# Performance work log

Measured on AMD Instinct MI355X. Metric: run time of the kernel, lower is better.

## Reference

```python
import jax, jax.numpy as jnp
import numpy as np

FEAT_STRIDE = 16
ANCHOR_SCALES = (8.0, 16.0, 32.0)
ANCHOR_RATIOS = (0.5, 1.0, 2.0)
NUM_ANCHORS = 9
PRE_NMS_TOP_N = 12000
POST_NMS_TOP_N = 300
NMS_THRESH = 0.7
POOLING_SIZE = 7
RPN_NEG_OVERLAP = 0.3
RPN_POS_OVERLAP = 0.7


def _generate_base_anchors(base_size=16):
    ratios = np.array(ANCHOR_RATIOS)
    scales = np.array(ANCHOR_SCALES)
    ctr = (base_size - 1) / 2.0
    size = float(base_size * base_size)
    ws = np.round(np.sqrt(size / ratios))
    hs = np.round(ws * ratios)
    ws = (ws[:, None] * scales[None, :]).ravel()  # order (ratio, scale)
    hs = (hs[:, None] * scales[None, :]).ravel()
    return np.stack([ctr - 0.5 * (ws - 1), ctr - 0.5 * (hs - 1),
                     ctr + 0.5 * (ws - 1), ctr + 0.5 * (hs - 1)], axis=1)


def _all_anchors(H, W):
    base = _generate_base_anchors()  # (A,4)
    sx = np.arange(W) * FEAT_STRIDE
    sy = np.arange(H) * FEAT_STRIDE
    sx, sy = np.meshgrid(sx, sy)  # (H,W)
    shifts = np.stack([sx.ravel(), sy.ravel(), sx.ravel(), sy.ravel()], axis=1)  # (H*W,4)
    anchors = (shifts[:, None, :] + base[None, :, :]).reshape(-1, 4)  # order (h,w,a)
    return jnp.asarray(anchors, dtype=jnp.float32)


def _conv(x, w, b):
    y = jax.lax.conv_general_dilated(x, w, (1, 1), 'SAME',
                                     dimension_numbers=('NCHW', 'OIHW', 'NCHW'))
    return y + b[None, :, None, None]


def _decode(anchors, deltas):
    w = anchors[:, 2] - anchors[:, 0] + 1.0
    h = anchors[:, 3] - anchors[:, 1] + 1.0
    cx = anchors[:, 0] + 0.5 * w
    cy = anchors[:, 1] + 0.5 * h
    pcx = deltas[:, 0] * w + cx
    pcy = deltas[:, 1] * h + cy
    pw = jnp.exp(deltas[:, 2]) * w
    ph = jnp.exp(deltas[:, 3]) * h
    return jnp.stack([pcx - 0.5 * pw, pcy - 0.5 * ph, pcx + 0.5 * pw, pcy + 0.5 * ph], axis=1)


def _encode(ex, gt):
    ew = ex[:, 2] - ex[:, 0] + 1.0
    eh = ex[:, 3] - ex[:, 1] + 1.0
    ecx = ex[:, 0] + 0.5 * ew
    ecy = ex[:, 1] + 0.5 * eh
    gw = gt[:, 2] - gt[:, 0] + 1.0
    gh = gt[:, 3] - gt[:, 1] + 1.0
    gcx = gt[:, 0] + 0.5 * gw
    gcy = gt[:, 1] + 0.5 * gh
    return jnp.stack([(gcx - ecx) / ew, (gcy - ecy) / eh,
                      jnp.log(gw / ew), jnp.log(gh / eh)], axis=1)


def _clip_boxes(b, im_h, im_w):
    return jnp.stack([jnp.clip(b[:, 0], 0.0, im_w - 1.0),
                      jnp.clip(b[:, 1], 0.0, im_h - 1.0),
                      jnp.clip(b[:, 2], 0.0, im_w - 1.0),
                      jnp.clip(b[:, 3], 0.0, im_h - 1.0)], axis=1)


def _iou_matrix(a, b):
    aa = (a[:, 2] - a[:, 0] + 1.0) * (a[:, 3] - a[:, 1] + 1.0)
    ba = (b[:, 2] - b[:, 0] + 1.0) * (b[:, 3] - b[:, 1] + 1.0)
    x1 = jnp.maximum(a[:, None, 0], b[None, :, 0])
    y1 = jnp.maximum(a[:, None, 1], b[None, :, 1])
    x2 = jnp.minimum(a[:, None, 2], b[None, :, 2])
    y2 = jnp.minimum(a[:, None, 3], b[None, :, 3])
    inter = jnp.maximum(x2 - x1 + 1.0, 0.0) * jnp.maximum(y2 - y1 + 1.0, 0.0)
    return inter / (aa[:, None] + ba[None, :] - inter)


def _nms(boxes, thresh, max_out):
    # boxes (N,4) already sorted by score descending; greedy NMS, fixed output size
    areas = (boxes[:, 2] - boxes[:, 0] + 1.0) * (boxes[:, 3] - boxes[:, 1] + 1.0)
    N = boxes.shape[0]

    def body(i, state):
        valid, keep = state
        idx = jnp.argmax(valid)  # first still-valid (highest score)
        has = valid[idx]
        b = boxes[idx]
        xx1 = jnp.maximum(b[0], boxes[:, 0])
        yy1 = jnp.maximum(b[1], boxes[:, 1])
        xx2 = jnp.minimum(b[2], boxes[:, 2])
        yy2 = jnp.minimum(b[3], boxes[:, 3])
        inter = jnp.maximum(xx2 - xx1 + 1.0, 0.0) * jnp.maximum(yy2 - yy1 + 1.0, 0.0)
        iou = inter / (areas[idx] + areas - inter)
        valid = jnp.where(has, valid & (iou <= thresh), valid)
        keep = keep.at[i].set(jnp.where(has, idx, 0).astype(jnp.int32))
        return valid, keep

    valid0 = jnp.ones((N,), dtype=bool)
    keep0 = jnp.zeros((max_out,), dtype=jnp.int32)
    _, keep = jax.lax.fori_loop(0, max_out, body, (valid0, keep0))
    return keep


def _roi_crop(feat, rois, P):
    # affine_grid + grid_sample (align_corners=True, zero padding), matching STRPN.pooling
    C, H, W = feat.shape[1], feat.shape[2], feat.shape[3]
    f = feat[0].reshape(C, H * W)
    R = rois.shape[0]
    x1 = rois[:, 1] / 16.0
    y1 = rois[:, 2] / 16.0
    x2 = rois[:, 3] / 16.0
    y2 = rois[:, 4] / 16.0
    t00 = (x2 - x1) / (W - 1)
    t02 = (x1 + x2 - W + 1) / (W - 1)
    t11 = (y2 - y1) / (H - 1)
    t12 = (y1 + y2 - H + 1) / (H - 1)
    lin = jnp.linspace(-1.0, 1.0, P)
    gx = jnp.broadcast_to(t00[:, None, None] * lin[None, None, :] + t02[:, None, None], (R, P, P))
    gy = jnp.broadcast_to(t11[:, None, None] * lin[None, :, None] + t12[:, None, None], (R, P, P))
    ix = (gx + 1.0) * 0.5 * (W - 1)
    iy = (gy + 1.0) * 0.5 * (H - 1)
    ix0 = jnp.floor(ix)
    iy0 = jnp.floor(iy)
    wx = ix - ix0
    wy = iy - iy0

    def gather(yi, xi, wgt):
        valid = (yi >= 0) & (yi < H) & (xi >= 0) & (xi < W)
        yc = jnp.clip(yi, 0, H - 1).astype(jnp.int32)
        xc = jnp.clip(xi, 0, W - 1).astype(jnp.int32)
        v = f[:, yc * W + xc]  # (C,R,P,P)
        return v * (wgt * valid)[None]

    out = (gather(iy0, ix0, (1 - wy) * (1 - wx)) + gather(iy0, ix0 + 1, (1 - wy) * wx)
           + gather(iy0 + 1, ix0, wy * (1 - wx)) + gather(iy0 + 1, ix0 + 1, wy * wx))
    return jnp.transpose(out, (1, 0, 2, 3))  # (R,C,P,P)


def _anchor_targets(anchors, gt_boxes, im_h, im_w):
    inside = ((anchors[:, 0] >= 0) & (anchors[:, 1] >= 0)
              & (anchors[:, 2] < im_w) & (anchors[:, 3] < im_h))
    ov = _iou_matrix(anchors, gt_boxes[:, :4])
    ov = jnp.where(inside[:, None], ov, -1.0)
    max_ov = ov.max(axis=1)
    argmax = ov.argmax(axis=1)
    gt_max = ov.max(axis=0)  # (G,)
    is_best = (ov == gt_max[None, :]).any(axis=1)
    labels = jnp.full(anchors.shape[:1], -1.0, dtype=jnp.float32)
    labels = jnp.where(inside & (max_ov < RPN_NEG_OVERLAP), 0.0, labels)
    labels = jnp.where(inside & is_best, 1.0, labels)
    labels = jnp.where(inside & (max_ov >= RPN_POS_OVERLAP), 1.0, labels)
    targets = _encode(anchors, gt_boxes[argmax, :4])
    pos = (labels == 1.0)
    ex = (labels >= 0.0)
    n_ex = jnp.maximum(ex.sum(), 1).astype(jnp.float32)
    in_w = pos[:, None].astype(jnp.float32)
    out_w = ex[:, None].astype(jnp.float32) / n_ex
    return labels, targets, in_w, out_w


def _forward(head_features, gt_boxes, im_info, rpn_w, rpn_b, cls_w, cls_b, bbox_w, bbox_b):
    A = NUM_ANCHORS
    H, W = head_features.shape[2], head_features.shape[3]
    anchors = _all_anchors(H, W)  # order (h,w,a)
    rpn = jax.nn.relu(_conv(head_features, rpn_w, rpn_b))
    cls_score = _conv(rpn, cls_w, cls_b)[0]   # (2A,H,W); channel layout cls*A + a
    bbox_pred = _conv(rpn, bbox_w, bbox_b)[0]  # (4A,H,W); channel layout a*4 + coord
    cls2 = cls_score.reshape(2, A, H, W)
    fg = jax.nn.softmax(cls2, axis=0)[1]  # (A,H,W)
    scores = jnp.transpose(fg, (1, 2, 0)).reshape(-1)  # (h,w,a)
    deltas = jnp.transpose(bbox_pred.reshape(A, 4, H, W), (2, 3, 0, 1)).reshape(-1, 4)
    im_h, im_w = im_info[0], im_info[1]
    proposals = _clip_boxes(_decode(anchors, deltas), im_h, im_w)
    _, order = jax.lax.top_k(scores, PRE_NMS_TOP_N)
    props = proposals[order]
    keep = _nms(props, NMS_THRESH, POST_NMS_TOP_N)
    sel = props[keep]
    rois = jnp.concatenate([jnp.zeros((POST_NMS_TOP_N, 1), sel.dtype), sel], axis=1)
    # RPN losses (anchor targets are numpy/constants in the original => stop_gradient)
    labels, tgt, iw, ow = jax.tree_util.tree_map(
        jax.lax.stop_gradient, _anchor_targets(anchors, gt_boxes, im_h, im_w))
    logits = jnp.transpose(cls2, (2, 3, 1, 0)).reshape(-1, 2)  # (h,w,a,2)
    logp = jax.nn.log_softmax(logits, axis=-1)
    mask = (labels >= 0).astype(logp.dtype)
    lbl = jnp.clip(labels, 0.0, 1.0).astype(jnp.int32)
    ce = -jnp.take_along_axis(logp, lbl[:, None], axis=1)[:, 0]
    cls_loss = jnp.sum(ce * mask) / jnp.maximum(mask.sum(), 1.0)
    sigma2 = 9.0  # sigma=3
    diff = iw * (deltas - tgt)
    ad = jnp.abs(diff)
    flag = (ad < 1.0 / sigma2).astype(diff.dtype)
    sl1 = flag * 0.5 * sigma2 * diff * diff + (1.0 - flag) * (ad - 0.5 / sigma2)
    box_loss = jnp.sum(ow * sl1)  # batch=1: sum over dims == mean over batch of per-image sums
    pooled = _roi_crop(head_features, jax.lax.stop_gradient(rois), POOLING_SIZE)
    return pooled, cls_loss, box_loss


def setup_inputs() -> dict:
    key = jax.random.key(0)
    ks = jax.random.split(key, 10)
    head_features = jax.random.normal(ks[0], (1, 1024, 96, 96), jnp.float32)
    G = 8
    x1 = jax.random.uniform(ks[1], (G,), minval=0.0, maxval=1100.0)
    y1 = jax.random.uniform(ks[2], (G,), minval=0.0, maxval=1000.0)
    bw = jax.random.uniform(ks[3], (G,), minval=50.0, maxval=300.0)
    bh = jax.random.uniform(ks[4], (G,), minval=100.0, maxval=450.0)
    gt_boxes = jnp.stack([x1, y1, jnp.minimum(x1 + bw, 1535.0),
                          jnp.minimum(y1 + bh, 1535.0), jnp.ones((G,))], axis=1).astype(jnp.float32)
    im_info = jnp.array([1536.0, 1536.0, 1.0], jnp.float32)
    rpn_w = jax.random.normal(ks[5], (512, 1024, 3, 3), jnp.float32) * 0.01
    rpn_b = jnp.zeros((512,), jnp.float32)
    cls_w = jax.random.normal(ks[6], (18, 512, 1, 1), jnp.float32) * 0.01
    cls_b = jnp.zeros((18,), jnp.float32)
    bbox_w = jax.random.normal(ks[7], (36, 512, 1, 1), jnp.float32) * 0.01
    bbox_b = jnp.zeros((36,), jnp.float32)
    return {"head_features": head_features, "gt_boxes": gt_boxes, "im_info": im_info,
            "rpn_w": rpn_w, "rpn_b": rpn_b, "cls_w": cls_w, "cls_b": cls_b,
            "bbox_w": bbox_w, "bbox_b": bbox_b}


def reference(head_features, gt_boxes, im_info, rpn_w, rpn_b, cls_w, cls_b, bbox_w, bbox_b):
    return _forward(head_features, gt_boxes, im_info, rpn_w, rpn_b, cls_w, cls_b, bbox_w, bbox_b)
```

## Files before the change

### kernel.cpp

```cpp
#include <hip/hip_runtime.h>
#include <stdint.h>

typedef unsigned int u32;
typedef unsigned long long u64;
typedef _Float16 f16x8 __attribute__((ext_vector_type(8)));
typedef float f32x4 __attribute__((ext_vector_type(4)));

#define HF 96
#define HW 9216
#define CIN 1024
#define CMID 512
#define NA 82944
#define PRE 12000
#define POST 300
#define NW 188
#define NBLK 324
#define OUT_POOL (POST*CIN*49)

__device__ __constant__ float BA[9][4] = {
  {-84.f,-40.f,99.f,55.f}, {-176.f,-88.f,191.f,103.f}, {-360.f,-184.f,375.f,199.f},
  {-56.f,-56.f,71.f,71.f}, {-120.f,-120.f,135.f,135.f}, {-248.f,-248.f,263.f,263.f},
  {-36.f,-80.f,51.f,95.f}, {-80.f,-168.f,95.f,183.f},  {-168.f,-344.f,183.f,359.f}
};

__device__ __forceinline__ u32 fkey(float f) {
  u32 u = __float_as_uint(f);
  return (u & 0x80000000u) ? ~u : (u | 0x80000000u);
}

__device__ __forceinline__ void gl_lds16(const void* g, void* l) {
  __builtin_amdgcn_global_load_lds((const __attribute__((address_space(1))) void*)g,
                                   (__attribute__((address_space(3))) void*)l, 16, 0, 0);
}

__global__ void prep_img(const float* __restrict__ feat, f16x8* __restrict__ img)
{
  __shared__ float ls[32][100];
  const int yy = blockIdx.x;
  const int kt = blockIdx.y;
  const int tid = threadIdx.x;
  const int y = yy - 1;
  const bool yok = (unsigned)y < 96u;
  if (yok) {
    for (int e = tid; e < 3072; e += 256) {
      const int ci = e / 96;
      const int x = e - ci * 96;
      ls[ci][x] = feat[(size_t)(kt*32 + ci)*HW + y*96 + x];
    }
  }
  __syncthreads();
  for (int idx = tid; idx < 784; idx += 256) {
    const int col = idx >> 3;
    const int q = idx & 7;
    const int x = col - 1;
    f16x8 val;
#pragma unroll
    for (int i=0;i<8;i++) val[i] = (_Float16)0.f;
    if (yok && (unsigned)x < 96u) {
#pragma unroll
      for (int i=0;i<8;i++) {
        const float v = ls[(q&3)*8 + i][x];
        if (q < 4) val[i] = (_Float16)v;
        else { const _Float16 hi = (_Float16)v; val[i] = (_Float16)((v - (float)hi)*1024.f); }
      }
    }
    const int sw = (col + 2*y) & 7;
    img[(size_t)((kt*98 + yy)*98 + col)*8 + (q ^ sw)] = val;
  }
}

__global__ void prep_w(const float* __restrict__ w, f16x8* __restrict__ wbuf)
{
  const int t = blockIdx.x*256 + threadIdx.x;
  const int co = t & 511;
  const int cic = t >> 9;
  const int kt = cic >> 2;
  const int kg = cic & 3;
  const float* wp = w + (size_t)co*9216 + cic*72;
#pragma unroll
  for (int tap=0; tap<9; ++tap) {
    f16x8 hv, lv;
#pragma unroll
    for (int i=0;i<8;i++) {
      const float v = wp[i*9 + tap] * 64.f;
      const _Float16 hi = (_Float16)v;
      hv[i] = hi;
      lv[i] = (_Float16)((v - (float)hi)*1024.f);
    }
    wbuf[(size_t)(((kt*9 + tap)*2 + 0)*4 + kg)*512 + co] = hv;
    wbuf[(size_t)(((kt*9 + tap)*2 + 1)*4 + kg)*512 + co] = lv;
  }
}

__global__ __launch_bounds__(128, 2) void rpn_conv_mfma(
    const f16x8* __restrict__ img, const f16x8* __restrict__ wbuf,
    const float* __restrict__ bias, float* __restrict__ out)
{
  __shared__ f16x8 in_s[2560];
  const int tid = threadIdx.x;
  const int lane = tid & 63;
  const int wv = tid >> 6;
  const int kgrp = lane >> 4;
  const int ln15 = lane & 15;
  const int x0 = blockIdx.x * 48;
  const int y  = blockIdx.y;
  const int co0 = blockIdx.z * 128 + wv * 64;

  int goff[10];
#pragma unroll
  for (int j=0;j<10;j++) {
    int s = j*128 + tid; if (s > 1199) s = 1199;
    const int row = s / 400;
    const int rem = s - row*400;
    goff[j] = ((y + row)*98 + x0 + (rem>>3))*8 + (rem & 7);
  }
  const int ldst0 = wv*64;

  int keyb[3];
#pragma unroll
  for (int pt=0; pt<3; ++pt) keyb[pt] = x0 + pt*16 + ln15 + 1 + 2*y;

  f32x4 acc1[4][3], acc2[4][3];
#pragma unroll
  for (int c=0;c<4;c++)
#pragma unroll
    for (int pt=0;pt<3;pt++) {
      acc1[c][pt] = (f32x4){0.f,0.f,0.f,0.f};
      acc2[c][pt] = (f32x4){0.f,0.f,0.f,0.f};
    }

  const int wlane = kgrp*512 + co0 + ln15;

#pragma unroll
  for (int j=0;j<10;j++) gl_lds16(img + goff[j], in_s + j*128 + ldst0);
  asm volatile("s_waitcnt vmcnt(0)" ::: "memory");
  __syncthreads();

  for (int kt = 0; kt < 32; ++kt) {
    const int cur = (kt & 1) * 1280;
    if (kt < 31) {
      const f16x8* kb = img + (size_t)(kt+1)*76832;
#pragma unroll
      for (int j=0;j<10;j++) gl_lds16(kb + goff[j], in_s + (1280 - cur) + j*128 + ldst0);
    }
    const f16x8* bs = in_s + cur;
#pragma unroll
    for (int t=0; t<9; ++t) {
      const int dy = t/3 - 1, dx = t%3 - 1;
      f16x8 af[4][2];
#pragma unroll
      for (int h=0;h<2;h++) {
        const size_t wb = (size_t)(((kt*9 + t)*2 + h)*2048) + wlane;
#pragma unroll
        for (int c=0;c<4;c++) af[c][h] = wbuf[wb + c*16];
      }
      f16x8 bf[3][2];
#pragma unroll
      for (int pt=0;pt<3;pt++) {
        const int key = (keyb[pt] + dx + 2*dy) & 7;
        const int base = ((dy+1)*50 + pt*16 + ln15 + dx + 1)*8;
#pragma unroll
        for (int h=0;h<2;h++)
          bf[pt][h] = bs[base + ((h*4 + kgrp) ^ key)];
      }
#pragma unroll
      for (int c=0;c<4;c++)
#pragma unroll
        for (int pt=0;pt<3;pt++) {
          acc1[c][pt] = __builtin_amdgcn_mfma_f32_16x16x32_f16(af[c][0], bf[pt][0], acc1[c][pt], 0,0,0);
          acc2[c][pt] = __builtin_amdgcn_mfma_f32_16x16x32_f16(af[c][0], bf[pt][1], acc2[c][pt], 0,0,0);
          acc2[c][pt] = __builtin_amdgcn_mfma_f32_16x16x32_f16(af[c][1], bf[pt][0], acc2[c][pt], 0,0,0);
        }
    }
    asm volatile("s_waitcnt vmcnt(0)" ::: "memory");
    __syncthreads();
  }

  const int pixb = y*96 + x0;
#pragma unroll
  for (int c=0;c<4;c++) {
#pragma unroll
    for (int i=0;i<4;i++) {
      const int co = co0 + c*16 + kgrp*4 + i;
      const float bb = bias[co];
#pragma unroll
      for (int pt=0;pt<3;pt++) {
        const float v = (acc1[c][pt][i] + acc2[c][pt][i]*(1.f/1024.f))*(1.f/64.f) + bb;
        out[(size_t)co*HW + pixb + pt*16 + ln15] = v > 0.f ? v : 0.f;
      }
    }
  }
}

__global__ void conv1x1p(const float* __restrict__ rpn,
    const float* __restrict__ cw, const float* __restrict__ bw,
    float* __restrict__ partial)
{
  const int hw = blockIdx.x * 256 + threadIdx.x;
  const int cg = blockIdx.y;
  const int ci0 = cg * 64;
  float accA[18], accB[36];
#pragma unroll
  for (int c=0;c<18;c++) accA[c]=0.f;
#pragma unroll
  for (int c=0;c<36;c++) accB[c]=0.f;
  for (int ci=ci0; ci<ci0+64; ++ci) {
    const float v = rpn[(size_t)ci*HW + hw];
#pragma unroll
    for (int c=0;c<18;c++) accA[c] = fmaf(v, cw[c*CMID+ci], accA[c]);
#pragma unroll
    for (int c=0;c<36;c++) accB[c] = fmaf(v, bw[c*CMID+ci], accB[c]);
  }
  float* p = partial + (size_t)cg*54*HW;
#pragma unroll
  for (int c=0;c<18;c++) p[(size_t)c*HW + hw] = accA[c];
#pragma unroll
  for (int c=0;c<36;c++) p[(size_t)(18+c)*HW + hw] = accB[c];
}

__global__ void conv1x1r(const float* __restrict__ partial,
    const float* __restrict__ cb, const float* __restrict__ bb,
    float* __restrict__ cls_out, float* __restrict__ bbox_out)
{
  const int o = blockIdx.x*256 + threadIdx.x;
  const int c = o / HW;
  const int hw = o - c*HW;
  float v = partial[o];
#pragma unroll
  for (int g=1; g<8; ++g) v += partial[(size_t)g*54*HW + o];
  if (c < 18) cls_out[(size_t)c*HW + hw] = v + cb[c];
  else        bbox_out[(size_t)(c-18)*HW + hw] = v + bb[c-18];
}

__global__ void score_decode_ov(const float* __restrict__ cls_out,
    const float* __restrict__ bbox_out, const float* __restrict__ im_info,
    const float* __restrict__ gt,
    u64* __restrict__ keys, float4* __restrict__ props, u32* __restrict__ hist10,
    float* __restrict__ ov, u32* __restrict__ gtmax)
{
#pragma clang fp contract(off)
  __shared__ u32 h[1024];
  __shared__ u32 lmax[8];
  const int tid = threadIdx.x;
  for (int i=tid;i<1024;i+=256) h[i]=0;
  if (tid < 8) lmax[tid] = 0u;
  __syncthreads();
  const int n = blockIdx.x*256 + tid;
  const int hw = n / 9;
  const int a  = n - hw*9;
  const int x = hw % HF, y = hw / HF;
  const float l0 = cls_out[a*HW + hw];
  const float l1 = cls_out[(9+a)*HW + hw];
  const float m = fmaxf(l0, l1);
  const float e0 = expf(l0 - m), e1 = expf(l1 - m);
  const float s = e1 / (e0 + e1);
  const u32 sb = __float_as_uint(s);
  keys[n] = ((u64)(~sb) << 32) | (u32)n;
  atomicAdd(&h[sb >> 22], 1u);

  const float ax1 = BA[a][0] + 16.f*(float)x;
  const float ay1 = BA[a][1] + 16.f*(float)y;
  const float ax2 = BA[a][2] + 16.f*(float)x;
  const float ay2 = BA[a][3] + 16.f*(float)y;
  const float aw = ax2 - ax1 + 1.f, ah = ay2 - ay1 + 1.f;
  const float cx = ax1 + 0.5f*aw,  cy = ay1 + 0.5f*ah;
  const float d0 = bbox_out[(a*4+0)*HW + hw];
  const float d1 = bbox_out[(a*4+1)*HW + hw];
  const float d2 = bbox_out[(a*4+2)*HW + hw];
  const float d3 = bbox_out[(a*4+3)*HW + hw];
  const float pcx = d0*aw + cx, pcy = d1*ah + cy;
  const float pw = expf(d2)*aw, ph = expf(d3)*ah;
  const float imh = im_info[0], imw = im_info[1];
  float bx1 = fminf(fmaxf(pcx - 0.5f*pw, 0.f), imw - 1.f);
  float by1 = fminf(fmaxf(pcy - 0.5f*ph, 0.f), imh - 1.f);
  float bx2 = fminf(fmaxf(pcx + 0.5f*pw, 0.f), imw - 1.f);
  float by2 = fminf(fmaxf(pcy + 0.5f*ph, 0.f), imh - 1.f);
  props[n] = make_float4(bx1, by1, bx2, by2);

  const bool inside = (ax1 >= 0.f) && (ay1 >= 0.f) && (ax2 < imw) && (ay2 < imh);
  const float aa = aw * ah;
#pragma unroll
  for (int j=0;j<8;j++) {
    const float g0=gt[j*5+0], g1=gt[j*5+1], g2=gt[j*5+2], g3=gt[j*5+3];
    const float ga = (g2-g0+1.f)*(g3-g1+1.f);
    const float xx1 = fmaxf(ax1,g0), yy1 = fmaxf(ay1,g1);
    const float xx2 = fminf(ax2,g2), yy2 = fminf(ay2,g3);
    const float inter = fmaxf(xx2-xx1+1.f,0.f)*fmaxf(yy2-yy1+1.f,0.f);
    const float iou = inter/(aa+ga-inter);
    const float o = inside ? iou : -1.f;
    ov[(size_t)n*8+j] = o;
    atomicMax(&lmax[j], fkey(o));
  }
  __syncthreads();
  for (int i=tid;i<1024;i+=256) if (h[i]) atomicAdd(&hist10[i], h[i]);
  if (tid < 8) atomicMax(&gtmax[tid], lmax[tid]);
}

__global__ void hist_scan1(const u32* __restrict__ hist10, u32* __restrict__ meta)
{
  __shared__ u32 c[1024];
  const int t = threadIdx.x;
  c[t] = hist10[t];
  __syncthreads();
  if (t == 0) {
    u32 cum = 0;
    int b = 1023;
    for (; b > 0; --b) {
      if (cum + c[b] >= PRE) break;
      cum += c[b];
    }
    meta[0] = (u32)b;
    meta[1] = cum;
  }
}

__global__ void refine_label(const u64* __restrict__ keys, const u32* __restrict__ meta,
                             u32* __restrict__ h64,
                             const float* __restrict__ ov, const u32* __restrict__ gtmax,
                             signed char* __restrict__ labels, signed char* __restrict__ amax,
                             int* __restrict__ exP)
{
  __shared__ u32 h[64];
  __shared__ int se[256];
  const int tid = threadIdx.x;
  if (tid < 64) h[tid] = 0;
  __syncthreads();
  const int n = blockIdx.x*256 + tid;
  const u32 sb = ~(u32)(keys[n] >> 32);
  if ((sb >> 22) == meta[0]) atomicAdd(&h[(sb >> 16) & 63], 1u);

  float best = -3.402823466e38f;
  int arg = 0;
  bool isbest = false;
#pragma unroll
  for (int j=0;j<8;j++) {
    const float o = ov[(size_t)n*8+j];
    if (o > best) { best = o; arg = j; }
    if (fkey(o) == gtmax[j]) isbest = true;
  }
  const bool inside = ov[(size_t)n*8+0] >= 0.f;
  int lab = -1;
  if (inside && best < 0.3f) lab = 0;
  if (inside && isbest) lab = 1;
  if (inside && best >= 0.7f) lab = 1;
  labels[n] = (signed char)lab;
  amax[n] = (signed char)arg;
  se[tid] = (lab >= 0) ? 1 : 0;
  __syncthreads();
  if (tid < 64 && h[tid]) atomicAdd(&h64[tid], h[tid]);
  for (int s=128; s>0; s>>=1) {
    if (tid < s) se[tid] += se[tid+s];
    __syncthreads();
  }
  if (tid==0) exP[blockIdx.x] = se[0];
}

__global__ void hist_scan2(const u32* __restrict__ h64, const u32* __restrict__ meta,
                           u32* __restrict__ thresh)
{
  u32 cum = meta[1];
  int s = 63;
  for (; s > 0; --s) { cum += h64[s]; if (cum >= PRE) break; }
  if (s == 0) cum += h64[0];
  thresh[0] = (meta[0] << 6) | (u32)s;
}

__global__ void collect_loss(const u64* __restrict__ keys, const u32* __restrict__ thresh,
                             u32* __restrict__ counter, u64* __restrict__ cand,
                             const float* __restrict__ cls_out, const float* __restrict__ bbox_out,
                             const float* __restrict__ gt, const signed char* __restrict__ labels,
                             const signed char* __restrict__ amax, float2* __restrict__ lossP)
{
#pragma clang fp contract(off)
  __shared__ float sce[256];
  __shared__ float sbx[256];
  const int tid = threadIdx.x;
  const int n = blockIdx.x*256 + tid;
  const u64 k = keys[n];
  const u32 sb = ~(u32)(k >> 32);
  if ((sb >> 16) >= thresh[0]) {
    u32 p = atomicAdd(counter, 1u);
    cand[p] = k;
  }
  const int hw = n/9, a = n - hw*9;
  const int lab = labels[n];
  float ce = 0.f, bx = 0.f;
  if (lab >= 0) {
    const float l0 = cls_out[a*HW+hw], l1 = cls_out[(9+a)*HW+hw];
    const float m = fmaxf(l0,l1);
    const float lse = m + logf(expf(l0-m)+expf(l1-m));
    ce = lse - (lab==1 ? l1 : l0);
  }
  if (lab == 1) {
    const int x = hw % HF, y = hw / HF;
    const float ax1 = BA[a][0]+16.f*(float)x, ay1 = BA[a][1]+16.f*(float)y;
    const float ax2 = BA[a][2]+16.f*(float)x, ay2 = BA[a][3]+16.f*(float)y;
    const float ew = ax2-ax1+1.f, eh = ay2-ay1+1.f;
    const float ecx = ax1+0.5f*ew, ecy = ay1+0.5f*eh;
    const int g = amax[n];
    const float g0=gt[g*5+0], g1=gt[g*5+1], g2=gt[g*5+2], g3=gt[g*5+3];
    const float gw = g2-g0+1.f, gh = g3-g1+1.f;
    const float gcx = g0+0.5f*gw, gcy = g1+0.5f*gh;
    float tgt[4];
    tgt[0] = (gcx-ecx)/ew;
    tgt[1] = (gcy-ecy)/eh;
    tgt[2] = logf(gw/ew);
    tgt[3] = logf(gh/eh);
#pragma unroll
    for (int j=0;j<4;j++) {
      const float d = bbox_out[(a*4+j)*HW+hw];
      const float diff = d - tgt[j];
      const float ad = fabsf(diff);
      bx += (ad < (1.0f/9.0f)) ? (4.5f*diff*diff) : (ad - 0.5f/9.0f);
    }
  }
  sce[tid]=ce; sbx[tid]=bx;
  __syncthreads();
  for (int s=128;s>0;s>>=1) {
    if (tid<s) { sce[tid]+=sce[tid+s]; sbx[tid]+=sbx[tid+s]; }
    __syncthreads();
  }
  if (tid==0) lossP[blockIdx.x] = make_float2(sce[0], sbx[0]);
}

__global__ void rank_partial(const u64* __restrict__ cand, const u32* __restrict__ counter,
                             u32* __restrict__ rankbuf)
{
  __shared__ u64 sk[256];
  const int M = (int)counter[0];
  if (blockIdx.x*256 >= M) return;
  const int i = blockIdx.x*256 + threadIdx.x;
  const u64 key = (i < M) ? cand[i] : ~0ull;
  const int chunk = ((M + 7)/8 + 255) & ~255;
  const int j0 = blockIdx.y*chunk;
  const int j1 = (j0 + chunk < M) ? (j0 + chunk) : M;
  int rank = 0;
  for (int t0 = j0; t0 < j1; t0 += 256) {
    const int j = t0 + threadIdx.x;
    sk[threadIdx.x] = (j < M) ? cand[j] : ~0ull;
    __syncthreads();
    const int lim = (j1 - t0 < 256) ? (j1 - t0) : 256;
    for (int k=0;k<lim;k++) rank += (sk[k] < key) ? 1 : 0;
    __syncthreads();
  }
  if (i < M && rank) atomicAdd(&rankbuf[i], (u32)rank);
}

__global__ void rank_scatter2(const u64* __restrict__ cand, const u32* __restrict__ counter,
                              const u32* __restrict__ rankbuf, const float4* __restrict__ props,
                              float4* __restrict__ sprops)
{
  const int M = (int)counter[0];
  const int i = blockIdx.x*256 + threadIdx.x;
  if (i >= M) return;
  const u32 r = rankbuf[i];
  if (r < PRE) sprops[r] = props[(u32)cand[i]];
}

__global__ void nms_mask(const float4* __restrict__ sp, u64* __restrict__ mask)
{
#pragma clang fp contract(off)
  if (blockIdx.x*64 + 63 < blockIdx.y*64) return;
  __shared__ float4 cb[64];
  __shared__ float  ca[64];
  const int c0 = blockIdx.x * 64;
  const int cend = min(64, PRE - c0);
  if ((int)threadIdx.x < cend) {
    float4 b = sp[c0 + threadIdx.x];
    cb[threadIdx.x] = b;
    ca[threadIdx.x] = (b.z-b.x+1.f)*(b.w-b.y+1.f);
  }
  __syncthreads();
  const int row = blockIdx.y*64 + threadIdx.x;
  if (row >= PRE) return;
  const float4 rb = sp[row];
  const float ra = (rb.z-rb.x+1.f)*(rb.w-rb.y+1.f);
  u64 bits = 0;
  for (int j=0;j<cend;j++) {
    const float4 c = cb[j];
    const float xx1 = fmaxf(rb.x, c.x), yy1 = fmaxf(rb.y, c.y);
    const float xx2 = fminf(rb.z, c.z), yy2 = fminf(rb.w, c.w);
    const float inter = fmaxf(xx2-xx1+1.f, 0.f) * fmaxf(yy2-yy1+1.f, 0.f);
    const float iou = inter / (ra + ca[j] - inter);
    if (iou > 0.7f) bits |= (1ull << j);
  }
  mask[(size_t)row*NW + blockIdx.x] = bits;
}

__global__ void fused_scan_tr(const u64* __restrict__ mask, const float4* __restrict__ sp,
                              float* __restrict__ rois,
                              const float2* __restrict__ lossP, const int* __restrict__ exP,
                              float* __restrict__ out,
                              const float* __restrict__ feat, float* __restrict__ featT, int doT)
{
  const int b = blockIdx.x;
  if (b == 0) {
    __shared__ int keep_s[POST];
    if (threadIdx.x < 64) {
      const int l = threadIdx.x;
      u64 v[4];
#pragma unroll
      for (int q=0;q<4;q++) {
        const int w = l*4+q;
        u64 val = 0;
        if (w < NW) { val = ~0ull; if (w == NW-1) val = (1ull<<32) - 1ull; }
        v[q] = val;
      }
      for (int it=0; it<POST; ++it) {
        const u64 nz = (v[0]|v[1]) | (v[2]|v[3]);
        const u64 bal = __ballot(nz != 0);
        int idx = -1;
        if (bal != 0) {
          const int src = __ffsll((unsigned long long)bal) - 1;
          int fi = 0;
          if (v[0])      fi = (l*4+0)*64 + __ffsll(v[0]) - 1;
          else if (v[1]) fi = (l*4+1)*64 + __ffsll(v[1]) - 1;
          else if (v[2]) fi = (l*4+2)*64 + __ffsll(v[2]) - 1;
          else if (v[3]) fi = (l*4+3)*64 + __ffsll(v[3]) - 1;
          idx = __shfl(fi, src);
        }
        if (l == 0) keep_s[it] = (idx < 0) ? 0 : idx;
        if (idx >= 0 && nz != 0) {
          const u64* mrow = mask + (size_t)idx*NW + l*4;
          v[0] &= ~mrow[0]; v[1] &= ~mrow[1]; v[2] &= ~mrow[2]; v[3] &= ~mrow[3];
        }
      }
    }
    __syncthreads();
    for (int i = threadIdx.x; i < POST; i += 256) {
      const float4 bb = sp[keep_s[i]];
      rois[i*5+0] = 0.f;
      rois[i*5+1] = bb.x; rois[i*5+2] = bb.y; rois[i*5+3] = bb.z; rois[i*5+4] = bb.w;
    }
  } else if (b == 1) {
    __shared__ float a[256];
    __shared__ float c[256];
    __shared__ int   e[256];
    const int t = threadIdx.x;
    float ax = 0.f, cx = 0.f; int ev = 0;
    if (t < NBLK) { float2 v = lossP[t]; ax = v.x; cx = v.y; ev = exP[t]; }
    if (t + 256 < NBLK) { float2 v = lossP[t+256]; ax += v.x; cx += v.y; ev += exP[t+256]; }
    a[t]=ax; c[t]=cx; e[t]=ev;
    __syncthreads();
    for (int s=128;s>0;s>>=1) {
      if (t<s) { a[t]+=a[t+s]; c[t]+=c[t+s]; e[t]+=e[t+s]; }
      __syncthreads();
    }
    if (t==0) {
      const float nex = (float)max(e[0], 1);
      out[OUT_POOL+0] = a[0] / nex;
      out[OUT_POOL+1] = c[0] / nex;
    }
  } else if (doT) {
    __shared__ float t[64][65];
    const int tt = b - 2;
    const int bxhw = (tt % 144)*64, byc = (tt / 144)*64;
    const int tid = threadIdx.x;
    const int l = tid & 63, g = tid >> 6;
#pragma unroll
    for (int i=0;i<16;i++) {
      const int cL = g + 4*i;
      t[cL][l] = feat[(size_t)(byc+cL)*HW + bxhw + l];
    }
    __syncthreads();
#pragma unroll
    for (int i=0;i<16;i++) {
      const int hwL = g + 4*i;
      featT[(size_t)(bxhw+hwL)*1024 + byc + l] = t[l][hwL];
    }
  }
}

struct __align__(16) Samp { int p0,p1,p2,p3; float w0,w1,w2,w3; };

__device__ __forceinline__ Samp make_samp(const float* __restrict__ rois, int r, int s)
{
#pragma clang fp contract(off)
  const int py = s / 7, px = s - py*7;
  const float x1 = rois[r*5+1] * 0.0625f;
  const float y1 = rois[r*5+2] * 0.0625f;
  const float x2 = rois[r*5+3] * 0.0625f;
  const float y2 = rois[r*5+4] * 0.0625f;
  const float t00 = (x2-x1)/95.f;
  const float t02 = (x1+x2-95.f)/95.f;
  const float t11 = (y2-y1)/95.f;
  const float t12 = (y1+y2-95.f)/95.f;
  const float lx = (float)(px-3)/3.f;
  const float ly = (float)(py-3)/3.f;
  const float gx = t00*lx + t02;
  const float gy = t11*ly + t12;
  const float ix = (gx+1.f)*0.5f*95.f;
  const float iy = (gy+1.f)*0.5f*95.f;
  const float ix0 = floorf(ix), iy0 = floorf(iy);
  const float wx = ix-ix0, wy = iy-iy0;
  const float xs[2] = {ix0, ix0+1.f};
  const float ys[2] = {iy0, iy0+1.f};
  const float wxs[2] = {1.f-wx, wx};
  const float wys[2] = {1.f-wy, wy};
  int pos[4]; float wt[4];
#pragma unroll
  for (int k=0;k<4;k++) {
    const int dy = k>>1, dx = k&1;
    const float yi = ys[dy], xi = xs[dx];
    const bool valid = (yi>=0.f)&&(yi<96.f)&&(xi>=0.f)&&(xi<96.f);
    const int yc = (int)fminf(fmaxf(yi,0.f),95.f);
    const int xc = (int)fminf(fmaxf(xi,0.f),95.f);
    pos[k] = yc*96+xc;
    wt[k] = wys[dy]*wxs[dx] * (valid?1.f:0.f);
  }
  Samp t;
  t.p0=pos[0]; t.p1=pos[1]; t.p2=pos[2]; t.p3=pos[3];
  t.w0=wt[0];  t.w1=wt[1];  t.w2=wt[2];  t.w3=wt[3];
  return t;
}

__global__ void roi_pool_coal(const float* __restrict__ featT, const float* __restrict__ rois,
                              float* __restrict__ out)
{
#pragma clang fp contract(off)
  __shared__ float st[49][257];
  __shared__ Samp sam[49];
  const int tid = threadIdx.x;
  const int r = blockIdx.x, cb = blockIdx.y;
  if (tid < 49) sam[tid] = make_samp(rois, r, tid);
  __syncthreads();
  const int c = cb*256 + tid;
  for (int s=0;s<49;s++) {
    const Samp t = sam[s];
    st[s][tid] = t.w0*featT[(size_t)t.p0*1024+c] + t.w1*featT[(size_t)t.p1*1024+c]
               + t.w2*featT[(size_t)t.p2*1024+c] + t.w3*featT[(size_t)t.p3*1024+c];
  }
  __syncthreads();
  float* ob = out + (size_t)r*50176 + cb*12544;
  for (int i=tid; i<12544; i+=256) {
    const int cL = i / 49, s = i - cL*49;
    ob[i] = st[s][cL];
  }
}

__global__ void roi_pool_gather(const float* __restrict__ feat, const float* __restrict__ rois,
                                float* __restrict__ out)
{
#pragma clang fp contract(off)
  const int o = blockIdx.x*256 + threadIdx.x;
  const int s  = o % 49;
  const int rc = o / 49;
  const int c = rc & (CIN-1);
  const int r = rc >> 10;
  const Samp t = make_samp(rois, r, s);
  const float* f = feat + (size_t)c*HW;
  out[o] = t.w0*f[t.p0] + t.w1*f[t.p1] + t.w2*f[t.p2] + t.w3*f[t.p3];
}

extern "C" void kernel_launch(void* const* d_in, const int* in_sizes, int n_in,
                              void* d_out, int out_size, void* d_ws, size_t ws_size,
                              hipStream_t stream)
{
  const float* feat    = (const float*)d_in[0];
  const float* gt      = (const float*)d_in[1];
  const float* im_info = (const float*)d_in[2];
  const float* rpn_w   = (const float*)d_in[3];
  const float* rpn_b   = (const float*)d_in[4];
  const float* cls_w   = (const float*)d_in[5];
  const float* cls_b   = (const float*)d_in[6];
  const float* bbox_w  = (const float*)d_in[7];
  const float* bbox_b  = (const float*)d_in[8];
  float* out = (float*)d_out;
  char* ws = (char*)d_ws;

  size_t off = 0;
  auto alloc = [&](size_t bytes) {
    size_t o = off;
    off = (off + bytes + 255) & ~(size_t)255;
    return o;
  };
  size_t o_counter = alloc(4);
  size_t o_gtmax   = alloc(32);
  size_t o_thresh  = alloc(4);
  size_t o_meta    = alloc(8);
  size_t o_h64     = alloc(256);
  size_t o_hist10  = alloc(1024*4);
  size_t o_rank    = alloc((size_t)NA*4);
  size_t zeroBytes = off;
  size_t o_cls  = alloc((size_t)18*HW*4);
  size_t o_bbox = alloc((size_t)36*HW*4);
  size_t o_rpn  = alloc((size_t)CMID*HW*4);
  size_t o_R = off;
  const size_t IMG_BYTES  = (size_t)32*98*98*8*16;
  const size_t WBUF_BYTES = (size_t)9*2*128*512*16;
  const size_t FEATT_BYTES= (size_t)HW*1024*4;
  size_t o_img  = o_R;
  size_t o_wbuf = o_R + ((IMG_BYTES + 255) & ~(size_t)255);
  size_t baseC_A = o_R + ((FEATT_BYTES + 255) & ~(size_t)255);
  auto phaseC = [&](size_t base, size_t* offs) {
    size_t co = base;
    auto ca = [&](size_t bytes) { size_t o = co; co = (co + bytes + 255) & ~(size_t)255; return o; };
    offs[0] = ca((size_t)8*54*HW*4);
    co = base;
    offs[1] = ca((size_t)NA*8);
    offs[2] = ca((size_t)NA*16);
    offs[3] = ca((size_t)NA*8);
    offs[4] = ca((size_t)PRE*16);
    offs[5] = ca((size_t)PRE*NW*8);
    offs[6] = ca((size_t)POST*5*4);
    offs[7] = ca((size_t)NA*8*4);
    offs[8] = ca((size_t)NA);
    offs[9] = ca((size_t)NA);
    offs[10]= ca((size_t)NBLK*4);
    offs[11]= ca((size_t)NBLK*8);
    size_t endC = co;
    size_t endB = base + (size_t)8*54*HW*4;
    return endC > endB ? endC : endB;
  };
  size_t offsA[12], offsB[12];
  size_t endA = phaseC(baseC_A, offsA);
  size_t convEnd = o_wbuf + WBUF_BYTES;
  size_t neededA = (endA > convEnd ? endA : convEnd);
  size_t endB = phaseC(o_R, offsB);
  (void)endB;
  const bool useT = (ws_size >= neededA);
  const size_t* offs = useT ? offsA : offsB;
  (void)in_sizes; (void)n_in; (void)out_size;

  hipMemsetAsync(ws, 0, zeroBytes, stream);

  f16x8* img      = (f16x8*)(ws + o_img);
  f16x8* wbuf     = (f16x8*)(ws + o_wbuf);
  float* featT    = (float*)(ws + o_R);
  float* partial  = (float*)(ws + offs[0]);
  float* rpn      = (float*)(ws + o_rpn);
  float* cls_out  = (float*)(ws + o_cls);
  float* bbox_out = (float*)(ws + o_bbox);
  u64*   keys     = (u64*)(ws + offs[1]);
  float4* props   = (float4*)(ws + offs[2]);
  u64*   cand     = (u64*)(ws + offs[3]);
  float4* sprops  = (float4*)(ws + offs[4]);
  u64*   maskp    = (u64*)(ws + offs[5]);
  float* rois     = (float*)(ws + offs[6]);
  float* ovp      = (float*)(ws + offs[7]);
  signed char* labels = (signed char*)(ws + offs[8]);
  signed char* amax   = (signed char*)(ws + offs[9]);
  int*    exP     = (int*)(ws + offs[10]);
  float2* lossP   = (float2*)(ws + offs[11]);
  u32* counter    = (u32*)(ws + o_counter);
  u32* gtmaxp     = (u32*)(ws + o_gtmax);
  u32* thresh     = (u32*)(ws + o_thresh);
  u32* metap      = (u32*)(ws + o_meta);
  u32* h64p       = (u32*)(ws + o_h64);
  u32* hist10     = (u32*)(ws + o_hist10);
  u32* rankbuf    = (u32*)(ws + o_rank);

  prep_img<<<dim3(98,32), 256, 0, stream>>>(feat, img);
  prep_w<<<256, 256, 0, stream>>>(rpn_w, wbuf);
  rpn_conv_mfma<<<dim3(2,96,4), 128, 0, stream>>>(img, wbuf, rpn_b, rpn);
  conv1x1p<<<dim3(36,8), 256, 0, stream>>>(rpn, cls_w, bbox_w, partial);
  conv1x1r<<<54*HW/256, 256, 0, stream>>>(partial, cls_b, bbox_b, cls_out, bbox_out);
  score_decode_ov<<<NBLK, 256, 0, stream>>>(cls_out, bbox_out, im_info, gt,
                                            keys, props, hist10, ovp, gtmaxp);
  hist_scan1<<<1, 1024, 0, stream>>>(hist10, metap);
  refine_label<<<NBLK, 256, 0, stream>>>(keys, metap, h64p, ovp, gtmaxp, labels, amax, exP);
  hist_scan2<<<1, 1, 0, stream>>>(h64p, metap, thresh);
  collect_loss<<<NBLK, 256, 0, stream>>>(keys, thresh, counter, cand,
                                         cls_out, bbox_out, gt, labels, amax, lossP);
  rank_partial<<<dim3(NBLK,8), 256, 0, stream>>>(cand, counter, rankbuf);
  rank_scatter2<<<NBLK, 256, 0, stream>>>(cand, counter, rankbuf, props, sprops);
  nms_mask<<<dim3(NW, NW), 64, 0, stream>>>(sprops, maskp);
  fused_scan_tr<<<2306, 256, 0, stream>>>(maskp, sprops, rois, lossP, exP, out,
                                          feat, featT, useT ? 1 : 0);
  if (useT) roi_pool_coal<<<dim3(POST,4), 256, 0, stream>>>(featT, rois, out);
  else      roi_pool_gather<<<OUT_POOL/256, 256, 0, stream>>>(feat, rois, out);
}
```

Measured before the change: 695.8 us.

## Remap conv blocks per XCD, prefetch weights, fuse threshold scan, prefetch NMS rows

The RPN conv kernel moves to a 1D grid whose block index is mapped so that blocks on the same XCD share output-channel tiles, which should improve L2 reuse of weights. Weight fragments for the next tap are loaded one step ahead into registers to hide global-load latency, at the cost of extra VGPRs. The single-thread hist_scan2 kernel is folded into collect_loss, with every block recomputing the threshold, which removes one launch. In the serial NMS scan, the mask row of the likely next keep is loaded speculatively into a sink to warm the cache, which may shorten the latency-bound loop.

```diff
diff --git a/kernel.cpp b/kernel.cpp
--- a/kernel.cpp
+++ b/kernel.cpp
@@ -97,14 +97,16 @@
     const float* __restrict__ bias, float* __restrict__ out)
 {
   __shared__ f16x8 in_s[2560];
+  const int bid = blockIdx.x;
+  const int xcd = bid & 7, seq = bid >> 3;
+  const int x0 = (seq & 1) * 48;
+  const int y  = (xcd & 1)*48 + (seq >> 1);
   const int tid = threadIdx.x;
   const int lane = tid & 63;
   const int wv = tid >> 6;
   const int kgrp = lane >> 4;
   const int ln15 = lane & 15;
-  const int x0 = blockIdx.x * 48;
-  const int y  = blockIdx.y;
-  const int co0 = blockIdx.z * 128 + wv * 64;
+  const int co0 = (xcd >> 1) * 128 + wv * 64;
 
   int goff[10];
 #pragma unroll
@@ -131,6 +133,13 @@
 
   const int wlane = kgrp*512 + co0 + ln15;
 
+  f16x8 afn[4][2];
+#pragma unroll
+  for (int h=0;h<2;h++)
+#pragma unroll
+    for (int c=0;c<4;c++)
+      afn[c][h] = wbuf[(size_t)(h*2048) + wlane + c*16];
+
 #pragma unroll
   for (int j=0;j<10;j++) gl_lds16(img + goff[j], in_s + j*128 + ldst0);
   asm volatile("s_waitcnt vmcnt(0)" ::: "memory");
@@ -146,14 +155,19 @@
     const f16x8* bs = in_s + cur;
 #pragma unroll
     for (int t=0; t<9; ++t) {
+      f16x8 af[4][2];
+#pragma unroll
+      for (int h=0;h<2;h++)
+#pragma unroll
+        for (int c=0;c<4;c++) af[c][h] = afn[c][h];
+      int Tn = kt*9 + t + 1; if (Tn > 287) Tn = 287;
+#pragma unroll
+      for (int h=0;h<2;h++)
+#pragma unroll
+        for (int c=0;c<4;c++)
+          afn[c][h] = wbuf[(size_t)(Tn*2 + h)*2048 + wlane + c*16];
+
       const int dy = t/3 - 1, dx = t%3 - 1;
-      f16x8 af[4][2];
-#pragma unroll
-      for (int h=0;h<2;h++) {
-        const size_t wb = (size_t)(((kt*9 + t)*2 + h)*2048) + wlane;
-#pragma unroll
-        for (int c=0;c<4;c++) af[c][h] = wbuf[wb + c*16];
-      }
       f16x8 bf[3][2];
 #pragma unroll
       for (int pt=0;pt<3;pt++) {
@@ -355,17 +369,8 @@
   if (tid==0) exP[blockIdx.x] = se[0];
 }
 
-__global__ void hist_scan2(const u32* __restrict__ h64, const u32* __restrict__ meta,
-                           u32* __restrict__ thresh)
-{
-  u32 cum = meta[1];
-  int s = 63;
-  for (; s > 0; --s) { cum += h64[s]; if (cum >= PRE) break; }
-  if (s == 0) cum += h64[0];
-  thresh[0] = (meta[0] << 6) | (u32)s;
-}
-
-__global__ void collect_loss(const u64* __restrict__ keys, const u32* __restrict__ thresh,
+__global__ void collect_loss(const u64* __restrict__ keys,
+                             const u32* __restrict__ meta, const u32* __restrict__ h64,
                              u32* __restrict__ counter, u64* __restrict__ cand,
                              const float* __restrict__ cls_out, const float* __restrict__ bbox_out,
                              const float* __restrict__ gt, const signed char* __restrict__ labels,
@@ -374,11 +379,20 @@
 #pragma clang fp contract(off)
   __shared__ float sce[256];
   __shared__ float sbx[256];
+  __shared__ u32 sthr;
   const int tid = threadIdx.x;
+  if (tid == 0) {
+    u32 cum = meta[1];
+    int s = 63;
+    for (; s > 0; --s) { cum += h64[s]; if (cum >= PRE) break; }
+    sthr = (meta[0] << 6) | (u32)s;
+  }
+  __syncthreads();
+  const u32 thr = sthr;
   const int n = blockIdx.x*256 + tid;
   const u64 k = keys[n];
   const u32 sb = ~(u32)(k >> 32);
-  if ((sb >> 16) >= thresh[0]) {
+  if ((sb >> 16) >= thr) {
     u32 p = atomicAdd(counter, 1u);
     cand[p] = k;
   }
@@ -499,6 +513,7 @@
     if (threadIdx.x < 64) {
       const int l = threadIdx.x;
       u64 v[4];
+      u64 sink = 0;
 #pragma unroll
       for (int q=0;q<4;q++) {
         const int w = l*4+q;
@@ -519,12 +534,37 @@
           else if (v[3]) fi = (l*4+3)*64 + __ffsll(v[3]) - 1;
           idx = __shfl(fi, src);
         }
+        int b1 = -1;
+        if (idx >= 0) {
+          u64 t0=v[0], t1=v[1], t2=v[2], t3=v[3];
+          if ((idx >> 8) == l) {
+            const int q = (idx >> 6) & 3;
+            const u64 mm = ~(1ull << (idx & 63));
+            if (q==0) t0 &= mm; else if (q==1) t1 &= mm; else if (q==2) t2 &= mm; else t3 &= mm;
+          }
+          const u64 nz2 = (t0|t1) | (t2|t3);
+          const u64 bal2 = __ballot(nz2 != 0);
+          if (bal2 != 0) {
+            const int s2 = __ffsll((unsigned long long)bal2) - 1;
+            int f2 = 0;
+            if (t0)      f2 = (l*4+0)*64 + __ffsll(t0) - 1;
+            else if (t1) f2 = (l*4+1)*64 + __ffsll(t1) - 1;
+            else if (t2) f2 = (l*4+2)*64 + __ffsll(t2) - 1;
+            else         f2 = (l*4+3)*64 + __ffsll(t3) - 1;
+            b1 = __shfl(f2, s2);
+          }
+        }
+        if (b1 >= 0 && l < 47) {
+          const u64* pr = mask + (size_t)b1*NW + l*4;
+          sink ^= pr[0] ^ pr[1] ^ pr[2] ^ pr[3];
+        }
         if (l == 0) keep_s[it] = (idx < 0) ? 0 : idx;
         if (idx >= 0 && nz != 0) {
           const u64* mrow = mask + (size_t)idx*NW + l*4;
           v[0] &= ~mrow[0]; v[1] &= ~mrow[1]; v[2] &= ~mrow[2]; v[3] &= ~mrow[3];
         }
       }
+      asm volatile("" :: "v"(sink));
     }
     __syncthreads();
     for (int i = threadIdx.x; i < POST; i += 256) {
@@ -676,7 +716,6 @@
   };
   size_t o_counter = alloc(4);
   size_t o_gtmax   = alloc(32);
-  size_t o_thresh  = alloc(4);
   size_t o_meta    = alloc(8);
   size_t o_h64     = alloc(256);
   size_t o_hist10  = alloc(1024*4);
@@ -744,7 +783,6 @@
   float2* lossP   = (float2*)(ws + offs[11]);
   u32* counter    = (u32*)(ws + o_counter);
   u32* gtmaxp     = (u32*)(ws + o_gtmax);
-  u32* thresh     = (u32*)(ws + o_thresh);
   u32* metap      = (u32*)(ws + o_meta);
   u32* h64p       = (u32*)(ws + o_h64);
   u32* hist10     = (u32*)(ws + o_hist10);
@@ -752,15 +790,14 @@
 
   prep_img<<<dim3(98,32), 256, 0, stream>>>(feat, img);
   prep_w<<<256, 256, 0, stream>>>(rpn_w, wbuf);
-  rpn_conv_mfma<<<dim3(2,96,4), 128, 0, stream>>>(img, wbuf, rpn_b, rpn);
+  rpn_conv_mfma<<<768, 128, 0, stream>>>(img, wbuf, rpn_b, rpn);
   conv1x1p<<<dim3(36,8), 256, 0, stream>>>(rpn, cls_w, bbox_w, partial);
   conv1x1r<<<54*HW/256, 256, 0, stream>>>(partial, cls_b, bbox_b, cls_out, bbox_out);
   score_decode_ov<<<NBLK, 256, 0, stream>>>(cls_out, bbox_out, im_info, gt,
                                             keys, props, hist10, ovp, gtmaxp);
   hist_scan1<<<1, 1024, 0, stream>>>(hist10, metap);
   refine_label<<<NBLK, 256, 0, stream>>>(keys, metap, h64p, ovp, gtmaxp, labels, amax, exP);
-  hist_scan2<<<1, 1, 0, stream>>>(h64p, metap, thresh);
-  collect_loss<<<NBLK, 256, 0, stream>>>(keys, thresh, counter, cand,
+  collect_loss<<<NBLK, 256, 0, stream>>>(keys, metap, h64p, counter, cand,
                                          cls_out, bbox_out, gt, labels, amax, lossP);
   rank_partial<<<dim3(NBLK,8), 256, 0, stream>>>(cand, counter, rankbuf);
   rank_scatter2<<<NBLK, 256, 0, stream>>>(cand, counter, rankbuf, props, sprops);
```

Result: slower. 799.7 us (+14.9%).
